# Kernel tuning notes

Measured on AMD Instinct MI355X. Metric: run time of the kernel, lower is better.

The kernel has to match this reference:

```python
import jax, jax.numpy as jnp
import numpy as np
import math

D_MODEL = 1024
N_HEADS = 16
D_K = 64
CHUNK_LEN = 64


def setup_inputs() -> dict:
    key = jax.random.key(0)
    ks = jax.random.split(key, 12)
    hd = N_HEADS * D_K
    s = 0.02
    return {
        'h': jax.random.normal(ks[0], (4, 2048, D_MODEL), jnp.float32),
        'e': jax.random.normal(ks[1], (4, 32, 2, 128, D_MODEL), jnp.float32),
        'Wq': jax.random.normal(ks[2], (D_MODEL, hd), jnp.float32) * s,
        'bq': jnp.zeros((hd,), jnp.float32),
        'Wk': jax.random.normal(ks[3], (D_MODEL, hd), jnp.float32) * s,
        'bk': jnp.zeros((hd,), jnp.float32),
        'Wv': jax.random.normal(ks[4], (D_MODEL, hd), jnp.float32) * s,
        'bv': jnp.zeros((hd,), jnp.float32),
        'Wo': jax.random.normal(ks[5], (hd, D_MODEL), jnp.float32) * s,
        'bo': jnp.zeros((D_MODEL,), jnp.float32),
        'gamma': jnp.ones((D_MODEL,), jnp.float32),
        'beta': jnp.zeros((D_MODEL,), jnp.float32),
    }


def reference(h, e, Wq, bq, Wk, bk, Wv, bv, Wo, bo, gamma, beta):
    b, chunks, neighbors, nlen, d_model = e.shape
    seq_len = h.shape[1]
    scale = 1.0 / math.sqrt(D_K)
    h_res = h
    # shift so chunk i attends to neighbors retrieved for chunk i
    hh = h[:, CHUNK_LEN - 1:]
    # layer norm
    mu = jnp.mean(hh, axis=-1, keepdims=True)
    var = jnp.mean(jnp.square(hh - mu), axis=-1, keepdims=True)
    hh = (hh - mu) / jnp.sqrt(var + 1e-5) * gamma + beta
    # pad to chunks * CHUNK_LEN
    pad = chunks * CHUNK_LEN - hh.shape[1]
    hh = jnp.pad(hh, ((0, 0), (0, pad), (0, 0)))
    hh = hh.reshape(b, chunks, CHUNK_LEN, d_model)
    q = (hh @ Wq + bq).reshape(b, chunks, CHUNK_LEN, N_HEADS, D_K)
    k = (e @ Wk + bk).reshape(b, chunks, neighbors, nlen, N_HEADS, D_K)
    v = (e @ Wv + bv).reshape(b, chunks, neighbors, nlen, N_HEADS, D_K)
    attn = jnp.einsum('bcihd,bcnjhd->bchinj', q, k) * scale  # [b,c,h,i,n,j]
    a_shape = attn.shape
    attn = jax.nn.softmax(attn.reshape(*a_shape[:-2], -1), axis=-1).reshape(a_shape)
    out = jnp.einsum('bchinj,bcnjhd->bcihd', attn, v)
    out = out.reshape(b, chunks * CHUNK_LEN, N_HEADS * D_K)
    out = out @ Wo + bo
    out = jnp.pad(out, ((0, 0), (CHUNK_LEN - 1, 0), (0, 0)))
    return out[:, :seq_len] + h_res
```

## Files before the change

### kernel.cpp

```cpp
#include <hip/hip_runtime.h>
#include <cstdint>
#include <cstddef>


typedef float f32x4 __attribute__((ext_vector_type(4)));
typedef __bf16 bf16x8 __attribute__((ext_vector_type(8)));

static __device__ __forceinline__ ushort f2bf(float f) {
  union { float f; uint32_t u; } x; x.f = f;
  uint32_t r = x.u + 0x7fffu + ((x.u >> 16) & 1u);
  return (ushort)(r >> 16);
}

static __device__ __forceinline__ bf16x8 ld_frag(const ushort* p) {
  union { uint4 u; bf16x8 v; } x;
  x.u = *(const uint4*)p;
  return x.v;
}

static __device__ __forceinline__ void gl2lds16(const ushort* g, ushort* l) {
  __builtin_amdgcn_global_load_lds(
      (const __attribute__((address_space(1))) void*)g,
      (__attribute__((address_space(3))) void*)l,
      16, 0, 0);
}

__global__ __launch_bounds__(256) void transpose_cast4(const float* __restrict__ Wq,
                                                       const float* __restrict__ Wk,
                                                       const float* __restrict__ Wv,
                                                       const float* __restrict__ Wo,
                                                       ushort* __restrict__ WqT,
                                                       ushort* __restrict__ WkvT,
                                                       ushort* __restrict__ WoT) {
  const float* W; ushort* WT;
  switch (blockIdx.z) {
    case 0:  W = Wq; WT = WqT; break;
    case 1:  W = Wk; WT = WkvT; break;
    case 2:  W = Wv; WT = WkvT + (size_t)1024 * 1024; break;
    default: W = Wo; WT = WoT; break;
  }
  __shared__ float tile[64][65];
  const int t = threadIdx.x;
  const int n0 = blockIdx.x * 64, k0 = blockIdx.y * 64;
#pragma unroll
  for (int i = 0; i < 4; ++i) {
    int lid = i * 256 + t;
    int r = lid >> 4, c4 = (lid & 15) * 4;
    float4 v = *(const float4*)&W[(size_t)(k0 + r) * 1024 + n0 + c4];
    tile[r][c4 + 0] = v.x; tile[r][c4 + 1] = v.y;
    tile[r][c4 + 2] = v.z; tile[r][c4 + 3] = v.w;
  }
  __syncthreads();
#pragma unroll
  for (int i = 0; i < 4; ++i) {
    int lid = i * 256 + t;
    int n = lid >> 4, k4 = (lid & 15) * 4;
    ushort4 o;
    o.x = f2bf(tile[k4 + 0][n]); o.y = f2bf(tile[k4 + 1][n]);
    o.z = f2bf(tile[k4 + 2][n]); o.w = f2bf(tile[k4 + 3][n]);
    *(ushort4*)&WT[(size_t)(n0 + n) * 1024 + k0 + k4] = o;
  }
}

__global__ __launch_bounds__(256) void cast_bf16(const float* __restrict__ x,
                                                 ushort* __restrict__ y) {
  const size_t i = ((size_t)blockIdx.x * 256 + threadIdx.x) * 8;
  float4 a = *(const float4*)&x[i];
  float4 b = *(const float4*)&x[i + 4];
  ushort o[8];
  o[0] = f2bf(a.x); o[1] = f2bf(a.y); o[2] = f2bf(a.z); o[3] = f2bf(a.w);
  o[4] = f2bf(b.x); o[5] = f2bf(b.y); o[6] = f2bf(b.z); o[7] = f2bf(b.w);
  *(uint4*)&y[i] = *(const uint4*)o;
}

__global__ __launch_bounds__(256) void ln_kernel(const float* __restrict__ h,
                                                 const float* __restrict__ gamma,
                                                 const float* __restrict__ beta,
                                                 ushort* __restrict__ hh) {
  const int bx = blockIdx.x;
  const int b = bx >> 11, s = bx & 2047;
  const int t = threadIdx.x;
  ushort* orow = hh + (size_t)(b * 2048 + s) * 1024;
  if (s >= 1985) {
    ushort4 z; z.x = 0; z.y = 0; z.z = 0; z.w = 0;
    *(ushort4*)&orow[t * 4] = z;
    return;
  }
  const float* xrow = h + (size_t)(b * 2048 + 63 + s) * 1024;
  float4 x = *(const float4*)&xrow[t * 4];
  float s1 = x.x + x.y + x.z + x.w;
  float s2 = x.x * x.x + x.y * x.y + x.z * x.z + x.w * x.w;
#pragma unroll
  for (int off = 32; off > 0; off >>= 1) {
    s1 += __shfl_xor(s1, off);
    s2 += __shfl_xor(s2, off);
  }
  __shared__ float a1[4], a2[4];
  if ((t & 63) == 0) { a1[t >> 6] = s1; a2[t >> 6] = s2; }
  __syncthreads();
  s1 = a1[0] + a1[1] + a1[2] + a1[3];
  s2 = a2[0] + a2[1] + a2[2] + a2[3];
  const float mu = s1 * (1.0f / 1024.0f);
  const float var = s2 * (1.0f / 1024.0f) - mu * mu;
  const float rstd = rsqrtf(var + 1e-5f);
  float4 g = *(const float4*)&gamma[t * 4];
  float4 be = *(const float4*)&beta[t * 4];
  ushort4 o;
  o.x = f2bf((x.x - mu) * rstd * g.x + be.x);
  o.y = f2bf((x.y - mu) * rstd * g.y + be.y);
  o.z = f2bf((x.z - mu) * rstd * g.z + be.z);
  o.w = f2bf((x.w - mu) * rstd * g.w + be.w);
  *(ushort4*)&orow[t * 4] = o;
}

template <int MODE, int NT>
__global__ __launch_bounds__(256) void gemm_bf16(const ushort* __restrict__ A,
                                                 const ushort* __restrict__ Bt,
                                                 const float* __restrict__ bias,
                                                 const float* __restrict__ bias2,
                                                 ushort* __restrict__ Cbf,
                                                 ushort* __restrict__ Vtg,
                                                 float* __restrict__ Cf,
                                                 const float* __restrict__ resid,
                                                 int mtiles, float scale,
                                                 int mrow_off) {
  if constexpr (MODE == 1) {
    if (blockIdx.x >= 512) {
      const int idx4 = (blockIdx.x - 512) * 256 + threadIdx.x;
      const int b = idx4 / 16128;
      const int rem = idx4 - b * 16128;
      const size_t o = (size_t)b * 2048 * 1024 + (size_t)rem * 4;
      *(float4*)&Cf[o] = *(const float4*)&resid[o];
      return;
    }
  }
  __shared__ __align__(16) ushort Alds[2][128 * 32];
  __shared__ __align__(16) ushort Blds[2][128 * 32];
  const int t = threadIdx.x;
  const int lane = t & 63, wave = t >> 6;
  const int quad = lane >> 4, l16 = lane & 15;

  const int L = blockIdx.x;
  const int xcd = L & 7, slot = L >> 3;
  const int nt = slot & (NT - 1);
  const int mt = xcd * (mtiles >> 3) + (slot / NT);
  const int m0 = mt * 128, n0 = nt * 128;

  const int srow = lane >> 2;
  const int scol = (lane & 3) * 8;
  const int c0 = wave * 2;
  const ushort* gA0 = A  + (size_t)(m0 + c0 * 16 + srow) * 1024 + scol;
  const ushort* gA1 = gA0 + 16 * 1024;
  const ushort* gB0 = Bt + (size_t)(n0 + c0 * 16 + srow) * 1024 + scol;
  const ushort* gB1 = gB0 + 16 * 1024;
  ushort* dA0 = &Alds[0][c0 * 512 + lane * 8];
  ushort* dA1 = dA0 + 512;
  ushort* dB0 = &Blds[0][c0 * 512 + lane * 8];
  ushort* dB1 = dB0 + 512;
  const ptrdiff_t SUB = 128 * 32;

  const int wrow = (wave >> 1) * 64, wcol = (wave & 1) * 64;
  const ushort* pA = &Alds[0][(wrow + l16) * 32 + quad * 8];
  const ushort* pB = &Blds[0][(wcol + l16) * 32 + quad * 8];

  f32x4 zero = {0.f, 0.f, 0.f, 0.f};
  f32x4 acc[4][4];
#pragma unroll
  for (int i = 0; i < 4; ++i)
#pragma unroll
    for (int j = 0; j < 4; ++j) acc[i][j] = zero;

  for (int kb = 0; kb < 16; ++kb) {
    const int ko = kb * 64;
    gl2lds16(gA0 + ko, dA0);         gl2lds16(gA1 + ko, dA1);
    gl2lds16(gA0 + ko + 32, dA0 + SUB); gl2lds16(gA1 + ko + 32, dA1 + SUB);
    gl2lds16(gB0 + ko, dB0);         gl2lds16(gB1 + ko, dB1);
    gl2lds16(gB0 + ko + 32, dB0 + SUB); gl2lds16(gB1 + ko + 32, dB1 + SUB);
    __syncthreads();
#pragma unroll
    for (int sub = 0; sub < 2; ++sub) {
      bf16x8 af[4], bfv[4];
#pragma unroll
      for (int i = 0; i < 4; ++i) af[i]  = ld_frag(pA + sub * SUB + i * 512);
#pragma unroll
      for (int j = 0; j < 4; ++j) bfv[j] = ld_frag(pB + sub * SUB + j * 512);
#pragma unroll
      for (int i = 0; i < 4; ++i)
#pragma unroll
        for (int j = 0; j < 4; ++j)
          acc[i][j] = __builtin_amdgcn_mfma_f32_16x16x32_bf16(af[i], bfv[j], acc[i][j], 0, 0, 0);
    }
    __syncthreads();
  }

#pragma unroll
  for (int mi = 0; mi < 4; ++mi)
#pragma unroll
    for (int mj = 0; mj < 4; ++mj) {
      const int cc = n0 + wcol + mj * 16 + l16;
      const int r0 = m0 + wrow + mi * 16 + quad * 4;
      if constexpr (MODE == 0) {
        const float bvb = bias[cc];
#pragma unroll
        for (int rr = 0; rr < 4; ++rr)
          Cbf[(size_t)(r0 + rr) * 1024 + cc] = f2bf((acc[mi][mj][rr] + bvb) * scale);
      } else {
        const float bvb = bias[cc];
#pragma unroll
        for (int rr = 0; rr < 4; ++rr) {
          const int r = r0 + rr;
          const int b = r >> 11, s = r & 2047;
          if (s < 1985) {
            const size_t o = (size_t)(b * 2048 + s + 63) * 1024 + cc;
            Cf[o] = acc[mi][mj][rr] + bvb + resid[o];
          }
        }
      }
    }
}

__global__ __launch_bounds__(512, 2) void gemm_kv256(const ushort* __restrict__ A,
                                                     const ushort* __restrict__ Bt,
                                                     const float* __restrict__ bk_,
                                                     const float* __restrict__ bv_,
                                                     ushort* __restrict__ Kout,
                                                     ushort* __restrict__ Vtg,
                                                     int mrow_off) {
  __shared__ __align__(16) ushort Alds[4 * 8192];
  __shared__ __align__(16) ushort Blds[4 * 8192];

  const int t = threadIdx.x;
  const int lane = t & 63, wave = t >> 6;
  const int wm = wave >> 2, wn = wave & 3;
  const int l16 = lane & 15, quad = lane >> 4;

  const int L = blockIdx.x;
  const int xcd = L & 7, slot = L >> 3;
  const int nt = slot & 7, mt = xcd * 8 + (slot >> 3);
  const int m0 = mt * 256, n0 = nt * 256;

  const int w2 = wave * 2;
  const int srow = lane >> 3;
  const int lanex = (lane & 7) ^ srow;
  const ushort* gA2 = A  + (size_t)(m0 + w2 * 8 + srow) * 1024 + lanex * 8;
  const ushort* gB2 = Bt + (size_t)(n0 + w2 * 8 + srow) * 1024 + lanex * 8;
  ushort* dA2 = Alds + w2 * 512 + lane * 8;
  ushort* dB2 = Blds + w2 * 512 + lane * 8;

  auto stage_a = [&](int ti, int hh) {
    const ushort* g = gA2 + (size_t)hh * 131072 + (size_t)ti * 64;
    ushort* d = dA2 + ((ti & 1) * 2 + hh) * 8192;
    gl2lds16(g, d);
    gl2lds16(g + 8192, d + 512);
  };
  auto stage_b = [&](int ti, int hh) {
    const ushort* g = gB2 + (size_t)hh * 131072 + (size_t)ti * 64;
    ushort* d = dB2 + ((ti & 1) * 2 + hh) * 8192;
    gl2lds16(g, d);
    gl2lds16(g + 8192, d + 512);
  };

  const int b2 = (l16 >> 2) & 1;
  const int qx = (quad ^ (l16 & 3)) << 3;
  const int kof0 = b2 << 5;
  const int kof1 = 32 - kof0;

  f32x4 zero = {0.f, 0.f, 0.f, 0.f};
  f32x4 acc[8][4];
#pragma unroll
  for (int i = 0; i < 8; ++i)
#pragma unroll
    for (int j = 0; j < 4; ++j) acc[i][j] = zero;

  stage_b(0, 0); stage_a(0, 0); stage_b(0, 1); stage_a(0, 1);
  stage_b(1, 0); stage_a(1, 0); stage_b(1, 1);
  asm volatile("s_waitcnt vmcnt(6)" ::: "memory");
  __builtin_amdgcn_s_barrier();

  bf16x8 a[4][2], b01[2][2], b23[2][2];

#pragma unroll 2
  for (int tt = 0; tt < 16; ++tt) {
    const int cur = tt & 1;
    const ushort* pa = Alds + (cur * 2 + wm) * 8192 + l16 * 64 + qx;
    const ushort* pb = Blds + (cur * 2 + (wn >> 1)) * 8192 +
                       ((wn & 1) * 64 + l16) * 64 + qx;

#pragma unroll
    for (int mi = 0; mi < 4; ++mi) {
      a[mi][0] = ld_frag(pa + mi * 1024 + kof0);
      a[mi][1] = ld_frag(pa + mi * 1024 + kof1);
    }
#pragma unroll
    for (int ni = 0; ni < 2; ++ni) {
      b01[ni][0] = ld_frag(pb + ni * 1024 + kof0);
      b01[ni][1] = ld_frag(pb + ni * 1024 + kof1);
    }
    if (tt < 15) stage_a(tt + 1, 1);
    __builtin_amdgcn_s_barrier();
    asm volatile("s_waitcnt lgkmcnt(0)" ::: "memory");
    __builtin_amdgcn_sched_barrier(0);
    __builtin_amdgcn_s_setprio(1);
#pragma unroll
    for (int mi = 0; mi < 4; ++mi)
#pragma unroll
      for (int ni = 0; ni < 2; ++ni) {
        acc[mi][ni] = __builtin_amdgcn_mfma_f32_16x16x32_bf16(a[mi][0], b01[ni][0], acc[mi][ni], 0, 0, 0);
        acc[mi][ni] = __builtin_amdgcn_mfma_f32_16x16x32_bf16(a[mi][1], b01[ni][1], acc[mi][ni], 0, 0, 0);
      }
    __builtin_amdgcn_s_setprio(0);
    __builtin_amdgcn_s_barrier();

#pragma unroll
    for (int ni = 0; ni < 2; ++ni) {
      b23[ni][0] = ld_frag(pb + (ni + 2) * 1024 + kof0);
      b23[ni][1] = ld_frag(pb + (ni + 2) * 1024 + kof1);
    }
    if (tt < 14) stage_b(tt + 2, 0);
    __builtin_amdgcn_s_barrier();
    asm volatile("s_waitcnt lgkmcnt(0)" ::: "memory");
    __builtin_amdgcn_sched_barrier(0);
    __builtin_amdgcn_s_setprio(1);
#pragma unroll
    for (int mi = 0; mi < 4; ++mi)
#pragma unroll
      for (int ni = 0; ni < 2; ++ni) {
        acc[mi][ni + 2] = __builtin_amdgcn_mfma_f32_16x16x32_bf16(a[mi][0], b23[ni][0], acc[mi][ni + 2], 0, 0, 0);
        acc[mi][ni + 2] = __builtin_amdgcn_mfma_f32_16x16x32_bf16(a[mi][1], b23[ni][1], acc[mi][ni + 2], 0, 0, 0);
      }
    __builtin_amdgcn_s_setprio(0);
    __builtin_amdgcn_s_barrier();

#pragma unroll
    for (int mi = 0; mi < 4; ++mi) {
      a[mi][0] = ld_frag(pa + (mi + 4) * 1024 + kof0);
      a[mi][1] = ld_frag(pa + (mi + 4) * 1024 + kof1);
    }
    if (tt < 14) stage_b(tt + 2, 1);
    __builtin_amdgcn_s_barrier();
    asm volatile("s_waitcnt lgkmcnt(0)" ::: "memory");
    __builtin_amdgcn_sched_barrier(0);
    __builtin_amdgcn_s_setprio(1);
#pragma unroll
    for (int mi = 0; mi < 4; ++mi)
#pragma unroll
      for (int ni = 0; ni < 2; ++ni) {
        acc[mi + 4][ni + 2] = __builtin_amdgcn_mfma_f32_16x16x32_bf16(a[mi][0], b23[ni][0], acc[mi + 4][ni + 2], 0, 0, 0);
        acc[mi + 4][ni + 2] = __builtin_amdgcn_mfma_f32_16x16x32_bf16(a[mi][1], b23[ni][1], acc[mi + 4][ni + 2], 0, 0, 0);
      }
    __builtin_amdgcn_s_setprio(0);
    __builtin_amdgcn_s_barrier();

    if (tt < 14) stage_a(tt + 2, 0);
    __builtin_amdgcn_s_barrier();
    __builtin_amdgcn_s_setprio(1);
#pragma unroll
    for (int mi = 0; mi < 4; ++mi)
#pragma unroll
      for (int ni = 0; ni < 2; ++ni) {
        acc[mi + 4][ni] = __builtin_amdgcn_mfma_f32_16x16x32_bf16(a[mi][0], b01[ni][0], acc[mi + 4][ni], 0, 0, 0);
        acc[mi + 4][ni] = __builtin_amdgcn_mfma_f32_16x16x32_bf16(a[mi][1], b01[ni][1], acc[mi + 4][ni], 0, 0, 0);
      }
    __builtin_amdgcn_s_setprio(0);
    if (tt < 15) {
      if (tt == 14) asm volatile("s_waitcnt vmcnt(0)" ::: "memory");
      else          asm volatile("s_waitcnt vmcnt(6)" ::: "memory");
      __builtin_amdgcn_s_barrier();
    }
  }

  const int rbase = m0 + wm * 128 + quad * 4;
  const int cbase = n0 + wn * 64 + l16;
  if (n0 < 1024) {
#pragma unroll
    for (int mi = 0; mi < 8; ++mi)
#pragma unroll
      for (int ni = 0; ni < 4; ++ni) {
        const int cc = cbase + ni * 16;
        const float bb = bk_[cc];
        const int r0 = rbase + mi * 16;
#pragma unroll
        for (int rr = 0; rr < 4; ++rr)
          Kout[(size_t)(r0 + rr) * 1024 + cc] = f2bf(acc[mi][ni][rr] + bb);
      }
  } else {
#pragma unroll
    for (int mi = 0; mi < 8; ++mi)
#pragma unroll
      for (int ni = 0; ni < 4; ++ni) {
        const int cv = cbase - 1024 + ni * 16;
        const int hh_ = cv >> 6, dd = cv & 63;
        const float bb = bv_[cv];
        const int gr0 = rbase + mi * 16 + mrow_off;
        const int bcl = gr0 >> 8, j0 = gr0 & 255;
        ushort4 o;
        o.x = f2bf(acc[mi][ni][0] + bb);
        o.y = f2bf(acc[mi][ni][1] + bb);
        o.z = f2bf(acc[mi][ni][2] + bb);
        o.w = f2bf(acc[mi][ni][3] + bb);
        *(ushort4*)&Vtg[(size_t)(bcl * 16 + hh_) * 16384 + dd * 256 + j0] = o;
      }
  }
}

__global__ __launch_bounds__(256, 2) void attn_kernel(const ushort* __restrict__ Qb,
                                                      const ushort* __restrict__ Kb,
                                                      const ushort* __restrict__ Vtg,
                                                      ushort* __restrict__ Ob) {
  __shared__ __align__(16) ushort Plds[4][4096];

  const int t = threadIdx.x;
  const int lane = t & 63, wave = t >> 6;
  const int quad = lane >> 4, l16 = lane & 15;
  const int hw = blockIdx.x * 4 + wave;
  const int hd = hw & 15, c = (hw >> 4) & 31, b = hw >> 9;

  const int qrow0 = b * 2048 + c * 64;
  const int kvrow0 = (b * 32 + c) * 256;
  const int colh = hd * 64;
  const ushort* vsrc = Vtg + ((size_t)((b * 32 + c) * 16 + hd)) * 16384;
  char* pw = (char*)&Plds[wave][0];
  const int swz = (l16 & 7) << 4;

  bf16x8 qf[4][2];
#pragma unroll
  for (int qq = 0; qq < 4; ++qq)
#pragma unroll
    for (int cc = 0; cc < 2; ++cc)
      qf[qq][cc] = ld_frag(&Qb[(size_t)(qrow0 + qq * 16 + l16) * 1024 +
                               colh + cc * 32 + quad * 8]);

  f32x4 zero = {0.f, 0.f, 0.f, 0.f};
  f32x4 Ot[4][4];
#pragma unroll
  for (int dd = 0; dd < 4; ++dd)
#pragma unroll
    for (int qq = 0; qq < 4; ++qq) Ot[dd][qq] = zero;
  float m[4], l[4];
#pragma unroll
  for (int qq = 0; qq < 4; ++qq) { m[qq] = -1e30f; l[qq] = 0.f; }

  for (int kb = 0; kb < 4; ++kb) {
    bf16x8 kf[4][2];
#pragma unroll
    for (int kk = 0; kk < 4; ++kk)
#pragma unroll
      for (int cc = 0; cc < 2; ++cc)
        kf[kk][cc] = ld_frag(&Kb[(size_t)(kvrow0 + kb * 64 + kk * 16 + l16) * 1024 +
                                 colh + cc * 32 + quad * 8]);

    f32x4 st[4][4];
#pragma unroll
    for (int kk = 0; kk < 4; ++kk)
#pragma unroll
      for (int qq = 0; qq < 4; ++qq) st[kk][qq] = zero;
#pragma unroll
    for (int cc = 0; cc < 2; ++cc)
#pragma unroll
      for (int kk = 0; kk < 4; ++kk)
#pragma unroll
        for (int qq = 0; qq < 4; ++qq)
          st[kk][qq] = __builtin_amdgcn_mfma_f32_16x16x32_bf16(kf[kk][cc], qf[qq][cc], st[kk][qq], 0, 0, 0);

    bf16x8 vf[4][2];
#pragma unroll
    for (int dd = 0; dd < 4; ++dd)
#pragma unroll
      for (int cc = 0; cc < 2; ++cc)
        vf[dd][cc] = ld_frag(&vsrc[(dd * 16 + l16) * 256 + kb * 64 + cc * 32 + quad * 8]);

#pragma unroll
    for (int qq = 0; qq < 4; ++qq) {
      float bm = st[0][qq][0];
#pragma unroll
      for (int kk = 0; kk < 4; ++kk)
#pragma unroll
        for (int rr = 0; rr < 4; ++rr) bm = fmaxf(bm, st[kk][qq][rr]);
      bm = fmaxf(bm, __shfl_xor(bm, 16));
      bm = fmaxf(bm, __shfl_xor(bm, 32));
      const float mn = fmaxf(m[qq], bm);
      const float sc = exp2f(m[qq] - mn);
      float bs = 0.f;
#pragma unroll
      for (int kk = 0; kk < 4; ++kk)
#pragma unroll
        for (int rr = 0; rr < 4; ++rr) {
          float p = exp2f(st[kk][qq][rr] - mn);
          st[kk][qq][rr] = p;
          bs += p;
        }
      bs += __shfl_xor(bs, 16);
      bs += __shfl_xor(bs, 32);
      l[qq] = l[qq] * sc + bs;
      m[qq] = mn;
#pragma unroll
      for (int dd = 0; dd < 4; ++dd) Ot[dd][qq] *= sc;
      const int rowb = (qq * 16 + l16) * 128;
#pragma unroll
      for (int kk = 0; kk < 4; ++kk) {
        uint32_t w0 = (uint32_t)f2bf(st[kk][qq][0]) | ((uint32_t)f2bf(st[kk][qq][1]) << 16);
        uint32_t w1 = (uint32_t)f2bf(st[kk][qq][2]) | ((uint32_t)f2bf(st[kk][qq][3]) << 16);
        const int byte = rowb + ((kk * 32 + quad * 8) ^ swz);
        *(uint32_t*)(pw + byte) = w0;
        *(uint32_t*)(pw + byte + 4) = w1;
      }
    }

#pragma unroll
    for (int qq = 0; qq < 4; ++qq)
#pragma unroll
      for (int cc = 0; cc < 2; ++cc) {
        const int byte = (qq * 16 + l16) * 128 + ((cc * 64 + quad * 16) ^ swz);
        bf16x8 pf = ld_frag((const ushort*)(pw + byte));
#pragma unroll
        for (int dd = 0; dd < 4; ++dd)
          Ot[dd][qq] = __builtin_amdgcn_mfma_f32_16x16x32_bf16(vf[dd][cc], pf, Ot[dd][qq], 0, 0, 0);
      }
  }

#pragma unroll
  for (int qq = 0; qq < 4; ++qq) {
    const float inv = 1.0f / l[qq];
    const int rowb = (qq * 16 + l16) * 128;
#pragma unroll
    for (int dd = 0; dd < 4; ++dd) {
      f32x4 v = Ot[dd][qq];
      uint32_t w0 = (uint32_t)f2bf(v[0] * inv) | ((uint32_t)f2bf(v[1] * inv) << 16);
      uint32_t w1 = (uint32_t)f2bf(v[2] * inv) | ((uint32_t)f2bf(v[3] * inv) << 16);
      const int byte = rowb + ((dd * 32 + quad * 8) ^ swz);
      *(uint32_t*)(pw + byte) = w0;
      *(uint32_t*)(pw + byte + 4) = w1;
    }
  }
#pragma unroll
  for (int p = 0; p < 8; ++p) {
    const int r = p * 8 + (lane >> 3);
    const int ch = lane & 7;
    const int byte = r * 128 + ((ch * 16) ^ ((r & 7) << 4));
    uint4 o = *(const uint4*)(pw + byte);
    *(uint4*)&Ob[(size_t)(qrow0 + r) * 1024 + colh + ch * 8] = o;
  }
}

extern "C" void kernel_launch(void* const* d_in, const int* in_sizes, int n_in,
                              void* d_out, int out_size, void* d_ws, size_t ws_size,
                              hipStream_t stream) {
  const float* h     = (const float*)d_in[0];
  const float* e     = (const float*)d_in[1];
  const float* Wq    = (const float*)d_in[2];
  const float* bq    = (const float*)d_in[3];
  const float* Wk    = (const float*)d_in[4];
  const float* bk    = (const float*)d_in[5];
  const float* Wv    = (const float*)d_in[6];
  const float* bv    = (const float*)d_in[7];
  const float* Wo    = (const float*)d_in[8];
  const float* bo    = (const float*)d_in[9];
  const float* gamma = (const float*)d_in[10];
  const float* beta  = (const float*)d_in[11];
  float* out = (float*)d_out;

  char* ws = (char*)d_ws;
  ushort* stg  = (ushort*)(ws + ((size_t)0 << 20));
  ushort* WqT  = (ushort*)(ws + ((size_t)32 << 20));
  ushort* WkvT = (ushort*)(ws + ((size_t)34 << 20));
  ushort* WoT  = (ushort*)(ws + ((size_t)38 << 20));
  ushort* Qb   = (ushort*)(ws + ((size_t)40 << 20));
  ushort* Kb   = (ushort*)(ws + ((size_t)56 << 20));
  ushort* VtG  = (ushort*)(ws + ((size_t)120 << 20));

  transpose_cast4<<<dim3(16, 16, 4), 256, 0, stream>>>(Wq, Wk, Wv, Wo, WqT, WkvT, WoT);

  ln_kernel<<<8192, 256, 0, stream>>>(h, gamma, beta, stg);

  gemm_bf16<0, 8><<<512, 256, 0, stream>>>(stg, WqT, bq, nullptr, Qb, nullptr,
                                           nullptr, nullptr, 64,
                                           0.125f * 1.4426950408889634f, 0);

  for (int half = 0; half < 2; ++half) {
    const size_t roff = (size_t)half * 16384 * 1024;
    cast_bf16<<<8192, 256, 0, stream>>>(e + roff, stg);
    gemm_kv256<<<512, 512, 0, stream>>>(stg, WkvT, bk, bv, Kb + roff,
                                        VtG, half * 16384);
  }

  attn_kernel<<<512, 256, 0, stream>>>(Qb, Kb, VtG, stg);

  gemm_bf16<1, 8><<<764, 256, 0, stream>>>(stg, WoT, bo, nullptr, nullptr, nullptr,
                                           out, h, 64, 1.0f, 0);
}
```

Before: 502.1 us.

## Fuse fp32-to-bf16 cast of neighbor embeddings into KV GEMM A-tile staging

```diff
diff --git a/kernel.cpp b/kernel.cpp
--- a/kernel.cpp
+++ b/kernel.cpp
@@ -60,17 +60,6 @@
     o.z = f2bf(tile[k4 + 2][n]); o.w = f2bf(tile[k4 + 3][n]);
     *(ushort4*)&WT[(size_t)(n0 + n) * 1024 + k0 + k4] = o;
   }
-}
-
-__global__ __launch_bounds__(256) void cast_bf16(const float* __restrict__ x,
-                                                 ushort* __restrict__ y) {
-  const size_t i = ((size_t)blockIdx.x * 256 + threadIdx.x) * 8;
-  float4 a = *(const float4*)&x[i];
-  float4 b = *(const float4*)&x[i + 4];
-  ushort o[8];
-  o[0] = f2bf(a.x); o[1] = f2bf(a.y); o[2] = f2bf(a.z); o[3] = f2bf(a.w);
-  o[4] = f2bf(b.x); o[5] = f2bf(b.y); o[6] = f2bf(b.z); o[7] = f2bf(b.w);
-  *(uint4*)&y[i] = *(const uint4*)o;
 }
 
 __global__ __launch_bounds__(256) void ln_kernel(const float* __restrict__ h,
@@ -219,7 +208,7 @@
     }
 }
 
-__global__ __launch_bounds__(512, 2) void gemm_kv256(const ushort* __restrict__ A,
+__global__ __launch_bounds__(512, 2) void gemm_kv256(const float* __restrict__ Ef,
                                                      const ushort* __restrict__ Bt,
                                                      const float* __restrict__ bk_,
                                                      const float* __restrict__ bv_,
@@ -242,16 +231,35 @@
   const int w2 = wave * 2;
   const int srow = lane >> 3;
   const int lanex = (lane & 7) ^ srow;
-  const ushort* gA2 = A  + (size_t)(m0 + w2 * 8 + srow) * 1024 + lanex * 8;
+  const float*  gAf = Ef + (size_t)(m0 + w2 * 8 + srow) * 1024 + lanex * 8;
   const ushort* gB2 = Bt + (size_t)(n0 + w2 * 8 + srow) * 1024 + lanex * 8;
   ushort* dA2 = Alds + w2 * 512 + lane * 8;
   ushort* dB2 = Blds + w2 * 512 + lane * 8;
 
-  auto stage_a = [&](int ti, int hh) {
-    const ushort* g = gA2 + (size_t)hh * 131072 + (size_t)ti * 64;
-    ushort* d = dA2 + ((ti & 1) * 2 + hh) * 8192;
-    gl2lds16(g, d);
-    gl2lds16(g + 8192, d + 512);
+  float4 areg[4][2];
+  auto issue_a = [&](int ti) {
+    const float* g = gAf + (size_t)ti * 64;
+#pragma unroll
+    for (int hh = 0; hh < 2; ++hh)
+#pragma unroll
+      for (int pp = 0; pp < 2; ++pp) {
+        const float* p = g + (size_t)(hh * 128 + pp * 8) * 1024;
+        areg[hh * 2 + pp][0] = *(const float4*)p;
+        areg[hh * 2 + pp][1] = *(const float4*)(p + 4);
+      }
+  };
+  auto write_a = [&](int ti) {
+    ushort* d = dA2 + ((ti & 1) * 2) * 8192;
+#pragma unroll
+    for (int hh = 0; hh < 2; ++hh)
+#pragma unroll
+      for (int pp = 0; pp < 2; ++pp) {
+        float4 x0 = areg[hh * 2 + pp][0], x1 = areg[hh * 2 + pp][1];
+        ushort o[8];
+        o[0] = f2bf(x0.x); o[1] = f2bf(x0.y); o[2] = f2bf(x0.z); o[3] = f2bf(x0.w);
+        o[4] = f2bf(x1.x); o[5] = f2bf(x1.y); o[6] = f2bf(x1.z); o[7] = f2bf(x1.w);
+        *(uint4*)(d + hh * 8192 + pp * 512) = *(const uint4*)o;
+      }
   };
   auto stage_b = [&](int ti, int hh) {
     const ushort* g = gB2 + (size_t)hh * 131072 + (size_t)ti * 64;
@@ -272,9 +280,12 @@
 #pragma unroll
     for (int j = 0; j < 4; ++j) acc[i][j] = zero;
 
-  stage_b(0, 0); stage_a(0, 0); stage_b(0, 1); stage_a(0, 1);
-  stage_b(1, 0); stage_a(1, 0); stage_b(1, 1);
-  asm volatile("s_waitcnt vmcnt(6)" ::: "memory");
+  issue_a(0);
+  stage_b(0, 0); stage_b(0, 1);
+  stage_b(1, 0); stage_b(1, 1);
+  asm volatile("s_waitcnt vmcnt(4)" ::: "memory");
+  write_a(0);
+  asm volatile("s_waitcnt lgkmcnt(0)" ::: "memory");
   __builtin_amdgcn_s_barrier();
 
   bf16x8 a[4][2], b01[2][2], b23[2][2];
@@ -296,7 +307,7 @@
       b01[ni][0] = ld_frag(pb + ni * 1024 + kof0);
       b01[ni][1] = ld_frag(pb + ni * 1024 + kof1);
     }
-    if (tt < 15) stage_a(tt + 1, 1);
+    if (tt < 15) issue_a(tt + 1);
     __builtin_amdgcn_s_barrier();
     asm volatile("s_waitcnt lgkmcnt(0)" ::: "memory");
     __builtin_amdgcn_sched_barrier(0);
@@ -351,7 +362,11 @@
     __builtin_amdgcn_s_setprio(0);
     __builtin_amdgcn_s_barrier();
 
-    if (tt < 14) stage_a(tt + 2, 0);
+    if (tt < 15) {
+      if (tt < 14) asm volatile("s_waitcnt vmcnt(4)" ::: "memory");
+      else         asm volatile("s_waitcnt vmcnt(0)" ::: "memory");
+      write_a(tt + 1);
+    }
     __builtin_amdgcn_s_barrier();
     __builtin_amdgcn_s_setprio(1);
 #pragma unroll
@@ -363,8 +378,7 @@
       }
     __builtin_amdgcn_s_setprio(0);
     if (tt < 15) {
-      if (tt == 14) asm volatile("s_waitcnt vmcnt(0)" ::: "memory");
-      else          asm volatile("s_waitcnt vmcnt(6)" ::: "memory");
+      asm volatile("s_waitcnt lgkmcnt(0)" ::: "memory");
       __builtin_amdgcn_s_barrier();
     }
   }
@@ -578,8 +592,7 @@
 
   for (int half = 0; half < 2; ++half) {
     const size_t roff = (size_t)half * 16384 * 1024;
-    cast_bf16<<<8192, 256, 0, stream>>>(e + roff, stg);
-    gemm_kv256<<<512, 512, 0, stream>>>(stg, WkvT, bk, bv, Kb + roff,
+    gemm_kv256<<<512, 512, 0, stream>>>(e + roff, WkvT, bk, bv, Kb + roff,
                                         VtG, half * 16384);
   }
 
```

After: 576.1 us. 1.15x slower.

## Merge weight transpose with layernorm and Q-projection with first e-cast

Applied to the files above, without the earlier changes.

```diff
diff --git a/kernel.cpp b/kernel.cpp
--- a/kernel.cpp
+++ b/kernel.cpp
@@ -25,65 +25,59 @@
       16, 0, 0);
 }
 
-__global__ __launch_bounds__(256) void transpose_cast4(const float* __restrict__ Wq,
-                                                       const float* __restrict__ Wk,
-                                                       const float* __restrict__ Wv,
-                                                       const float* __restrict__ Wo,
-                                                       ushort* __restrict__ WqT,
-                                                       ushort* __restrict__ WkvT,
-                                                       ushort* __restrict__ WoT) {
-  const float* W; ushort* WT;
-  switch (blockIdx.z) {
-    case 0:  W = Wq; WT = WqT; break;
-    case 1:  W = Wk; WT = WkvT; break;
-    case 2:  W = Wv; WT = WkvT + (size_t)1024 * 1024; break;
-    default: W = Wo; WT = WoT; break;
-  }
+__global__ __launch_bounds__(256) void prep_kernel(const float* __restrict__ Wq,
+                                                   const float* __restrict__ Wk,
+                                                   const float* __restrict__ Wv,
+                                                   const float* __restrict__ Wo,
+                                                   const float* __restrict__ h,
+                                                   const float* __restrict__ gamma,
+                                                   const float* __restrict__ beta,
+                                                   ushort* __restrict__ WqT,
+                                                   ushort* __restrict__ WkvT,
+                                                   ushort* __restrict__ WoT,
+                                                   ushort* __restrict__ lnout) {
   __shared__ float tile[64][65];
+  __shared__ float a1[4], a2[4];
   const int t = threadIdx.x;
-  const int n0 = blockIdx.x * 64, k0 = blockIdx.y * 64;
-#pragma unroll
-  for (int i = 0; i < 4; ++i) {
-    int lid = i * 256 + t;
-    int r = lid >> 4, c4 = (lid & 15) * 4;
-    float4 v = *(const float4*)&W[(size_t)(k0 + r) * 1024 + n0 + c4];
-    tile[r][c4 + 0] = v.x; tile[r][c4 + 1] = v.y;
-    tile[r][c4 + 2] = v.z; tile[r][c4 + 3] = v.w;
-  }
-  __syncthreads();
-#pragma unroll
-  for (int i = 0; i < 4; ++i) {
-    int lid = i * 256 + t;
-    int n = lid >> 4, k4 = (lid & 15) * 4;
-    ushort4 o;
-    o.x = f2bf(tile[k4 + 0][n]); o.y = f2bf(tile[k4 + 1][n]);
-    o.z = f2bf(tile[k4 + 2][n]); o.w = f2bf(tile[k4 + 3][n]);
-    *(ushort4*)&WT[(size_t)(n0 + n) * 1024 + k0 + k4] = o;
-  }
-}
-
-__global__ __launch_bounds__(256) void cast_bf16(const float* __restrict__ x,
-                                                 ushort* __restrict__ y) {
-  const size_t i = ((size_t)blockIdx.x * 256 + threadIdx.x) * 8;
-  float4 a = *(const float4*)&x[i];
-  float4 b = *(const float4*)&x[i + 4];
-  ushort o[8];
-  o[0] = f2bf(a.x); o[1] = f2bf(a.y); o[2] = f2bf(a.z); o[3] = f2bf(a.w);
-  o[4] = f2bf(b.x); o[5] = f2bf(b.y); o[6] = f2bf(b.z); o[7] = f2bf(b.w);
-  *(uint4*)&y[i] = *(const uint4*)o;
-}
-
-__global__ __launch_bounds__(256) void ln_kernel(const float* __restrict__ h,
-                                                 const float* __restrict__ gamma,
-                                                 const float* __restrict__ beta,
-                                                 ushort* __restrict__ hh) {
   const int bx = blockIdx.x;
-  const int b = bx >> 11, s = bx & 2047;
-  const int t = threadIdx.x;
-  ushort* orow = hh + (size_t)(b * 2048 + s) * 1024;
+
+  if (bx < 1024) {
+    const int z = bx >> 8, rem = bx & 255;
+    const int n0 = (rem & 15) * 64, k0 = (rem >> 4) * 64;
+    const float* W; ushort* WT;
+    switch (z) {
+      case 0:  W = Wq; WT = WqT; break;
+      case 1:  W = Wk; WT = WkvT; break;
+      case 2:  W = Wv; WT = WkvT + (size_t)1024 * 1024; break;
+      default: W = Wo; WT = WoT; break;
+    }
+#pragma unroll
+    for (int i = 0; i < 4; ++i) {
+      int lid = i * 256 + t;
+      int r = lid >> 4, c4 = (lid & 15) * 4;
+      float4 v = *(const float4*)&W[(size_t)(k0 + r) * 1024 + n0 + c4];
+      tile[r][c4 + 0] = v.x; tile[r][c4 + 1] = v.y;
+      tile[r][c4 + 2] = v.z; tile[r][c4 + 3] = v.w;
+    }
+    __syncthreads();
+#pragma unroll
+    for (int i = 0; i < 4; ++i) {
+      int lid = i * 256 + t;
+      int n = lid >> 4, k4 = (lid & 15) * 4;
+      ushort4 o;
+      o.x = f2bf(tile[k4 + 0][n]); o.y = f2bf(tile[k4 + 1][n]);
+      o.z = f2bf(tile[k4 + 2][n]); o.w = f2bf(tile[k4 + 3][n]);
+      *(ushort4*)&WT[(size_t)(n0 + n) * 1024 + k0 + k4] = o;
+    }
+    return;
+  }
+
+  const int bx2 = bx - 1024;
+  const int b = bx2 >> 11, s = bx2 & 2047;
+  ushort* orow = lnout + (size_t)(b * 2048 + s) * 1024;
   if (s >= 1985) {
-    ushort4 z; z.x = 0; z.y = 0; z.z = 0; z.w = 0;
-    *(ushort4*)&orow[t * 4] = z;
+    ushort4 z4; z4.x = 0; z4.y = 0; z4.z = 0; z4.w = 0;
+    *(ushort4*)&orow[t * 4] = z4;
     return;
   }
   const float* xrow = h + (size_t)(b * 2048 + 63 + s) * 1024;
@@ -95,7 +89,6 @@
     s1 += __shfl_xor(s1, off);
     s2 += __shfl_xor(s2, off);
   }
-  __shared__ float a1[4], a2[4];
   if ((t & 63) == 0) { a1[t >> 6] = s1; a2[t >> 6] = s2; }
   __syncthreads();
   s1 = a1[0] + a1[1] + a1[2] + a1[3];
@@ -113,26 +106,33 @@
   *(ushort4*)&orow[t * 4] = o;
 }
 
-template <int MODE, int NT>
-__global__ __launch_bounds__(256) void gemm_bf16(const ushort* __restrict__ A,
-                                                 const ushort* __restrict__ Bt,
-                                                 const float* __restrict__ bias,
-                                                 const float* __restrict__ bias2,
-                                                 ushort* __restrict__ Cbf,
-                                                 ushort* __restrict__ Vtg,
-                                                 float* __restrict__ Cf,
-                                                 const float* __restrict__ resid,
-                                                 int mtiles, float scale,
-                                                 int mrow_off) {
-  if constexpr (MODE == 1) {
-    if (blockIdx.x >= 512) {
-      const int idx4 = (blockIdx.x - 512) * 256 + threadIdx.x;
-      const int b = idx4 / 16128;
-      const int rem = idx4 - b * 16128;
-      const size_t o = (size_t)b * 2048 * 1024 + (size_t)rem * 4;
-      *(float4*)&Cf[o] = *(const float4*)&resid[o];
-      return;
-    }
+__global__ __launch_bounds__(256) void cast_bf16(const float* __restrict__ x,
+                                                 ushort* __restrict__ y) {
+  const size_t i = ((size_t)blockIdx.x * 256 + threadIdx.x) * 8;
+  float4 a = *(const float4*)&x[i];
+  float4 b = *(const float4*)&x[i + 4];
+  ushort o[8];
+  o[0] = f2bf(a.x); o[1] = f2bf(a.y); o[2] = f2bf(a.z); o[3] = f2bf(a.w);
+  o[4] = f2bf(b.x); o[5] = f2bf(b.y); o[6] = f2bf(b.z); o[7] = f2bf(b.w);
+  *(uint4*)&y[i] = *(const uint4*)o;
+}
+
+__global__ __launch_bounds__(256) void qproj_cast(const ushort* __restrict__ A,
+                                                  const ushort* __restrict__ Bt,
+                                                  const float* __restrict__ bias,
+                                                  ushort* __restrict__ Cbf,
+                                                  float scale,
+                                                  const float* __restrict__ ex,
+                                                  ushort* __restrict__ ey) {
+  if (blockIdx.x >= 512) {
+    const size_t i = ((size_t)(blockIdx.x - 512) * 256 + threadIdx.x) * 8;
+    float4 a = *(const float4*)&ex[i];
+    float4 b = *(const float4*)&ex[i + 4];
+    ushort o[8];
+    o[0] = f2bf(a.x); o[1] = f2bf(a.y); o[2] = f2bf(a.z); o[3] = f2bf(a.w);
+    o[4] = f2bf(b.x); o[5] = f2bf(b.y); o[6] = f2bf(b.z); o[7] = f2bf(b.w);
+    *(uint4*)&ey[i] = *(const uint4*)o;
+    return;
   }
   __shared__ __align__(16) ushort Alds[2][128 * 32];
   __shared__ __align__(16) ushort Blds[2][128 * 32];
@@ -142,8 +142,8 @@
 
   const int L = blockIdx.x;
   const int xcd = L & 7, slot = L >> 3;
-  const int nt = slot & (NT - 1);
-  const int mt = xcd * (mtiles >> 3) + (slot / NT);
+  const int nt = slot & 7;
+  const int mt = xcd * 8 + (slot >> 3);
   const int m0 = mt * 128, n0 = nt * 128;
 
   const int srow = lane >> 2;
@@ -199,21 +199,101 @@
     for (int mj = 0; mj < 4; ++mj) {
       const int cc = n0 + wcol + mj * 16 + l16;
       const int r0 = m0 + wrow + mi * 16 + quad * 4;
-      if constexpr (MODE == 0) {
-        const float bvb = bias[cc];
-#pragma unroll
-        for (int rr = 0; rr < 4; ++rr)
-          Cbf[(size_t)(r0 + rr) * 1024 + cc] = f2bf((acc[mi][mj][rr] + bvb) * scale);
-      } else {
-        const float bvb = bias[cc];
-#pragma unroll
-        for (int rr = 0; rr < 4; ++rr) {
-          const int r = r0 + rr;
-          const int b = r >> 11, s = r & 2047;
-          if (s < 1985) {
-            const size_t o = (size_t)(b * 2048 + s + 63) * 1024 + cc;
-            Cf[o] = acc[mi][mj][rr] + bvb + resid[o];
-          }
+      const float bvb = bias[cc];
+#pragma unroll
+      for (int rr = 0; rr < 4; ++rr)
+        Cbf[(size_t)(r0 + rr) * 1024 + cc] = f2bf((acc[mi][mj][rr] + bvb) * scale);
+    }
+}
+
+template <int MODE, int NT>
+__global__ __launch_bounds__(256) void gemm_bf16(const ushort* __restrict__ A,
+                                                 const ushort* __restrict__ Bt,
+                                                 const float* __restrict__ bias,
+                                                 float* __restrict__ Cf,
+                                                 const float* __restrict__ resid,
+                                                 int mtiles) {
+  if (blockIdx.x >= 512) {
+    const int idx4 = (blockIdx.x - 512) * 256 + threadIdx.x;
+    const int b = idx4 / 16128;
+    const int rem = idx4 - b * 16128;
+    const size_t o = (size_t)b * 2048 * 1024 + (size_t)rem * 4;
+    *(float4*)&Cf[o] = *(const float4*)&resid[o];
+    return;
+  }
+  __shared__ __align__(16) ushort Alds[2][128 * 32];
+  __shared__ __align__(16) ushort Blds[2][128 * 32];
+  const int t = threadIdx.x;
+  const int lane = t & 63, wave = t >> 6;
+  const int quad = lane >> 4, l16 = lane & 15;
+
+  const int L = blockIdx.x;
+  const int xcd = L & 7, slot = L >> 3;
+  const int nt = slot & (NT - 1);
+  const int mt = xcd * (mtiles >> 3) + (slot / NT);
+  const int m0 = mt * 128, n0 = nt * 128;
+
+  const int srow = lane >> 2;
+  const int scol = (lane & 3) * 8;
+  const int c0 = wave * 2;
+  const ushort* gA0 = A  + (size_t)(m0 + c0 * 16 + srow) * 1024 + scol;
+  const ushort* gA1 = gA0 + 16 * 1024;
+  const ushort* gB0 = Bt + (size_t)(n0 + c0 * 16 + srow) * 1024 + scol;
+  const ushort* gB1 = gB0 + 16 * 1024;
+  ushort* dA0 = &Alds[0][c0 * 512 + lane * 8];
+  ushort* dA1 = dA0 + 512;
+  ushort* dB0 = &Blds[0][c0 * 512 + lane * 8];
+  ushort* dB1 = dB0 + 512;
+  const ptrdiff_t SUB = 128 * 32;
+
+  const int wrow = (wave >> 1) * 64, wcol = (wave & 1) * 64;
+  const ushort* pA = &Alds[0][(wrow + l16) * 32 + quad * 8];
+  const ushort* pB = &Blds[0][(wcol + l16) * 32 + quad * 8];
+
+  f32x4 zero = {0.f, 0.f, 0.f, 0.f};
+  f32x4 acc[4][4];
+#pragma unroll
+  for (int i = 0; i < 4; ++i)
+#pragma unroll
+    for (int j = 0; j < 4; ++j) acc[i][j] = zero;
+
+  for (int kb = 0; kb < 16; ++kb) {
+    const int ko = kb * 64;
+    gl2lds16(gA0 + ko, dA0);         gl2lds16(gA1 + ko, dA1);
+    gl2lds16(gA0 + ko + 32, dA0 + SUB); gl2lds16(gA1 + ko + 32, dA1 + SUB);
+    gl2lds16(gB0 + ko, dB0);         gl2lds16(gB1 + ko, dB1);
+    gl2lds16(gB0 + ko + 32, dB0 + SUB); gl2lds16(gB1 + ko + 32, dB1 + SUB);
+    __syncthreads();
+#pragma unroll
+    for (int sub = 0; sub < 2; ++sub) {
+      bf16x8 af[4], bfv[4];
+#pragma unroll
+      for (int i = 0; i < 4; ++i) af[i]  = ld_frag(pA + sub * SUB + i * 512);
+#pragma unroll
+      for (int j = 0; j < 4; ++j) bfv[j] = ld_frag(pB + sub * SUB + j * 512);
+#pragma unroll
+      for (int i = 0; i < 4; ++i)
+#pragma unroll
+        for (int j = 0; j < 4; ++j)
+          acc[i][j] = __builtin_amdgcn_mfma_f32_16x16x32_bf16(af[i], bfv[j], acc[i][j], 0, 0, 0);
+    }
+    __syncthreads();
+  }
+
+#pragma unroll
+  for (int mi = 0; mi < 4; ++mi)
+#pragma unroll
+    for (int mj = 0; mj < 4; ++mj) {
+      const int cc = n0 + wcol + mj * 16 + l16;
+      const int r0 = m0 + wrow + mi * 16 + quad * 4;
+      const float bvb = bias[cc];
+#pragma unroll
+      for (int rr = 0; rr < 4; ++rr) {
+        const int r = r0 + rr;
+        const int b = r >> 11, s = r & 2047;
+        if (s < 1985) {
+          const size_t o = (size_t)(b * 2048 + s + 63) * 1024 + cc;
+          Cf[o] = acc[mi][mj][rr] + bvb + resid[o];
         }
       }
     }
@@ -568,23 +648,19 @@
   ushort* Kb   = (ushort*)(ws + ((size_t)56 << 20));
   ushort* VtG  = (ushort*)(ws + ((size_t)120 << 20));
 
-  transpose_cast4<<<dim3(16, 16, 4), 256, 0, stream>>>(Wq, Wk, Wv, Wo, WqT, WkvT, WoT);
-
-  ln_kernel<<<8192, 256, 0, stream>>>(h, gamma, beta, stg);
-
-  gemm_bf16<0, 8><<<512, 256, 0, stream>>>(stg, WqT, bq, nullptr, Qb, nullptr,
-                                           nullptr, nullptr, 64,
-                                           0.125f * 1.4426950408889634f, 0);
-
-  for (int half = 0; half < 2; ++half) {
-    const size_t roff = (size_t)half * 16384 * 1024;
-    cast_bf16<<<8192, 256, 0, stream>>>(e + roff, stg);
-    gemm_kv256<<<512, 512, 0, stream>>>(stg, WkvT, bk, bv, Kb + roff,
-                                        VtG, half * 16384);
-  }
+  prep_kernel<<<9216, 256, 0, stream>>>(Wq, Wk, Wv, Wo, h, gamma, beta,
+                                        WqT, WkvT, WoT, VtG);
+
+  qproj_cast<<<8704, 256, 0, stream>>>(VtG, WqT, bq, Qb,
+                                       0.125f * 1.4426950408889634f,
+                                       e, stg);
+
+  gemm_kv256<<<512, 512, 0, stream>>>(stg, WkvT, bk, bv, Kb, VtG, 0);
+  cast_bf16<<<8192, 256, 0, stream>>>(e + (size_t)16384 * 1024, stg);
+  gemm_kv256<<<512, 512, 0, stream>>>(stg, WkvT, bk, bv,
+                                      Kb + (size_t)16384 * 1024, VtG, 16384);
 
   attn_kernel<<<512, 256, 0, stream>>>(Qb, Kb, VtG, stg);
 
-  gemm_bf16<1, 8><<<764, 256, 0, stream>>>(stg, WoT, bo, nullptr, nullptr, nullptr,
-                                           out, h, 64, 1.0f, 0);
-}
+  gemm_bf16<1, 8><<<764, 256, 0, stream>>>(stg, WoT, bo, out, h, 64);
+}
```

After: 498.2 us. Within noise of the previous version (-0.8%).
